# Kernel tuning notes

Hardware: AMD Instinct MI355X
Metric: run time of the kernel (lower is better)

Reference implementation:

```python
import jax, jax.numpy as jnp
import numpy as np

HIDDEN = 1024
HEADS = 16
HEAD_DIM = HIDDEN // HEADS
SCALE = 1.0 / (HEAD_DIM ** 0.5)


def setup_inputs() -> dict:
    key = jax.random.key(0)
    k1, k2, k3 = jax.random.split(key, 3)
    B, S = 2, 2048
    x = jax.random.normal(k1, (B, S, HIDDEN), dtype=jnp.float32)
    # torch Linear weights: (out_features, in_features), y = x @ W.T
    qkv_w = jax.random.normal(k2, (3 * HIDDEN, HIDDEN), dtype=jnp.float32) * (HIDDEN ** -0.5)
    out_w = jax.random.normal(k3, (HIDDEN, HIDDEN), dtype=jnp.float32) * (HIDDEN ** -0.5)
    return {"x": x, "qkv_w": qkv_w, "out_w": out_w}


def reference(x, qkv_w, out_w):
    B, S, H = x.shape
    qkv = jnp.einsum('bsh,oh->bso', x, qkv_w)  # [B,S,3H]
    q, k, v = jnp.split(qkv, 3, axis=-1)
    def heads(t):
        return t.reshape(B, S, HEADS, HEAD_DIM).transpose(0, 2, 1, 3)  # [B,nh,S,hd]
    q, k, v = heads(q), heads(k), heads(v)
    scores = jnp.einsum('bhqd,bhkd->bhqk', q, k) * SCALE  # [B,nh,S,S]
    attn = jax.nn.softmax(scores, axis=-1)
    out = jnp.einsum('bhqk,bhkd->bhqd', attn, v)  # [B,nh,S,hd]
    out = out.transpose(0, 2, 1, 3).reshape(B, S, H)
    return jnp.einsum('bsh,oh->bso', out, out_w)
```

## Files before the change

kernel.cpp:

```cpp
#include <hip/hip_runtime.h>
#include <hip/hip_bf16.h>

#define BB 2
#define SS 2048
#define HH 1024
#define NH 16
#define HD 64
#define MM (BB * SS)
#define N_QKV (3 * HH)
#define KK HH

typedef __attribute__((ext_vector_type(8))) short short8;
typedef __attribute__((ext_vector_type(4))) float floatx4;
typedef __attribute__((ext_vector_type(16))) float floatx16;

#define MFMA16(a, b, c) __builtin_amdgcn_mfma_f32_16x16x32_bf16(a, b, c, 0, 0, 0)
#define MFMA32(a, b, c) __builtin_amdgcn_mfma_f32_32x32x16_bf16(a, b, c, 0, 0, 0)

__device__ __forceinline__ unsigned short f2bf(float f) {
  unsigned int u = __builtin_bit_cast(unsigned int, f);
  u += 0x7FFFu + ((u >> 16) & 1u);
  return (unsigned short)(u >> 16);
}

__device__ __forceinline__ float fexp2(float x) {
#if __has_builtin(__builtin_amdgcn_exp2f)
  return __builtin_amdgcn_exp2f(x);
#else
  float r; asm("v_exp_f32 %0, %1" : "=v"(r) : "v"(x)); return r;
#endif
}

__device__ __forceinline__ unsigned int pack2e(float lo, float hi) {
  unsigned int a = __builtin_bit_cast(unsigned int, lo) + 0x8000u;
  unsigned int b = __builtin_bit_cast(unsigned int, hi) + 0x8000u;
  return __builtin_amdgcn_perm(b, a, 0x07060302u);
}

__device__ __forceinline__ unsigned int cvtpk(float lo, float hi) {
  unsigned int r;
  asm("v_cvt_pk_bf16_f32 %0, %1, %2" : "=v"(r) : "v"(lo), "v"(hi));
  return r;
}

__device__ __forceinline__ uint4 cvt8pk(float4 lo, float4 hi) {
  uint4 u;
  u.x = cvtpk(lo.x, lo.y);
  u.y = cvtpk(lo.z, lo.w);
  u.z = cvtpk(hi.x, hi.y);
  u.w = cvtpk(hi.z, hi.w);
  return u;
}

__device__ __forceinline__ void gload_lds16(const void* g, void* l) {
  __builtin_amdgcn_global_load_lds((const __attribute__((address_space(1))) void*)g,
                                   (__attribute__((address_space(3))) void*)l,
                                   16, 0, 0);
}

__global__ __launch_bounds__(256) void cast_g(const float* __restrict__ s,
                                              unsigned short* __restrict__ d) {
  size_t i = (size_t)blockIdx.x * 256 + threadIdx.x;
  float4 lo = *(const float4*)(s + i * 8);
  float4 hi = *(const float4*)(s + i * 8 + 4);
  *(uint4*)(d + i * 8) = cvt8pk(lo, hi);
}

template <int BPRE>
__global__ __launch_bounds__(256) void gemm_qkv(const unsigned short* __restrict__ Xb,
                                                const float* __restrict__ Wf,
                                                const unsigned short* __restrict__ Wb,
                                                unsigned short* __restrict__ qb,
                                                unsigned short* __restrict__ kb,
                                                unsigned short* __restrict__ vtb) {
  __shared__ __attribute__((aligned(16))) unsigned short As[128 * 32];
  __shared__ __attribute__((aligned(16))) unsigned short Bs[128 * 32];
  const int tid = threadIdx.x;
  const int wave = tid >> 6, lane = tid & 63;
  const int quad = lane >> 4, lc = lane & 15;
  const int m0 = blockIdx.y * 128, n0 = blockIdx.x * 128;
  const int wm = (wave >> 1) * 64, wn = (wave & 1) * 64;
  const int sr = tid >> 2, sc = (tid & 3) * 8;

  floatx4 acc[4][4];
#pragma unroll
  for (int i = 0; i < 4; i++)
#pragma unroll
    for (int j = 0; j < 4; j++) acc[i][j] = (floatx4){0.f, 0.f, 0.f, 0.f};

  const unsigned short* Axp = Xb + (size_t)(m0 + sr) * KK + sc;
  unsigned short* AsD = As + wave * 512;
  unsigned short* BsD = Bs + wave * 512;

  const unsigned short* Bxp = nullptr;
  const float* Bg = nullptr;
  float4 b0l, b0h, b1l, b1h;
  unsigned short* BsW = Bs + wave * 512 + lane * 8;
  if constexpr (BPRE) {
    Bxp = Wb + (size_t)(n0 + sr) * KK + sc;
  } else {
    Bg = Wf + (size_t)(n0 + sr) * KK + sc;
    b0l = *(const float4*)(Bg);                    b0h = *(const float4*)(Bg + 4);
    b1l = *(const float4*)(Bg + (size_t)64 * KK);  b1h = *(const float4*)(Bg + (size_t)64 * KK + 4);
  }

  for (int it = 0; it < KK / 32; ++it) {
    const int k0 = it * 32;
    __syncthreads();
    gload_lds16(Axp + k0, AsD);
    gload_lds16(Axp + (size_t)64 * KK + k0, AsD + 2048);
    if constexpr (BPRE) {
      gload_lds16(Bxp + k0, BsD);
      gload_lds16(Bxp + (size_t)64 * KK + k0, BsD + 2048);
    } else {
      *(uint4*)(BsW) = cvt8pk(b0l, b0h);
      *(uint4*)(BsW + 2048) = cvt8pk(b1l, b1h);
      if (it + 1 < KK / 32) {
        b0l = *(const float4*)(Bg + k0 + 32);                    b0h = *(const float4*)(Bg + k0 + 36);
        b1l = *(const float4*)(Bg + k0 + 32 + (size_t)64 * KK);  b1h = *(const float4*)(Bg + k0 + 36 + (size_t)64 * KK);
      }
    }
    __syncthreads();
    short8 af[4], bf[4];
#pragma unroll
    for (int i = 0; i < 4; i++) {
      af[i] = *(const short8*)(As + (wm + i * 16 + lc) * 32 + quad * 8);
      bf[i] = *(const short8*)(Bs + (wn + i * 16 + lc) * 32 + quad * 8);
    }
#pragma unroll
    for (int i = 0; i < 4; i++)
#pragma unroll
      for (int j = 0; j < 4; j++) acc[i][j] = MFMA16(af[i], bf[j], acc[i][j]);
  }

  const float QSCALE = 0.125f * 1.44269504f;
#pragma unroll
  for (int j = 0; j < 4; j++) {
    int n = n0 + wn + j * 16 + lc;
#pragma unroll
    for (int i = 0; i < 4; i++) {
      int mbase = m0 + wm + i * 16 + quad * 4;
      int b = mbase >> 11;
      int s0 = mbase & 2047;
      if (n < HH) {
        int h = n >> 6, d = n & 63;
#pragma unroll
        for (int r = 0; r < 4; r++)
          qb[(((size_t)(b * NH + h) * SS + s0 + r) * HD) + d] = f2bf(acc[i][j][r] * QSCALE);
      } else if (n < 2 * HH) {
        int n2 = n - HH; int h = n2 >> 6, d = n2 & 63;
#pragma unroll
        for (int r = 0; r < 4; r++)
          kb[(((size_t)(b * NH + h) * SS + s0 + r) * HD) + d] = f2bf(acc[i][j][r]);
      } else {
        int n2 = n - 2 * HH; int h = n2 >> 6, d = n2 & 63;
        ushort4 p;
        p.x = f2bf(acc[i][j][0]); p.y = f2bf(acc[i][j][1]);
        p.z = f2bf(acc[i][j][2]); p.w = f2bf(acc[i][j][3]);
        *(ushort4*)(vtb + ((size_t)(b * NH + h) * HD + d) * SS + s0) = p;
      }
    }
  }
}

__device__ __forceinline__ int co(int row, int c16) {
  return row * 64 + ((c16 ^ ((row ^ (row >> 3)) & 7)) << 3);
}

__global__ __launch_bounds__(256, 2) void attn_kernel(const unsigned short* __restrict__ qg,
                                                      const unsigned short* __restrict__ kg,
                                                      const unsigned short* __restrict__ vtg,
                                                      unsigned short* __restrict__ og) {
  __shared__ __attribute__((aligned(16))) unsigned short Sall[16384];
  unsigned short* Qs = Sall;
  unsigned short* Ks = Sall + 8192;
  unsigned short* Vs = Sall + 12288;

  const int tid = threadIdx.x;
  const int w = tid >> 6, lane = tid & 63;
  const int hl = lane >> 5, c = lane & 31;
  const int q0 = blockIdx.x * 128;
  const int head = blockIdx.y, b = blockIdx.z;

  const unsigned short* qbase = qg + (size_t)(b * NH + head) * SS * HD;
  const unsigned short* kbase = kg + (size_t)(b * NH + head) * SS * HD;
  const unsigned short* vbase = vtg + (size_t)(b * NH + head) * HD * SS;

  {
    int row = tid >> 3, cc = tid & 7;
#pragma unroll
    for (int s = 0; s < 4; s++)
      *(uint4*)(Qs + co(row + 32 * s, cc)) =
          *(const uint4*)(qbase + (size_t)(q0 + row + 32 * s) * HD + cc * 8);
  }

  const int frow = tid >> 3, fc = tid & 7;
  uint4 k0r = *(const uint4*)(kbase + (size_t)frow * HD + fc * 8);
  uint4 k1r = *(const uint4*)(kbase + (size_t)(frow + 32) * HD + fc * 8);
  uint4 v0r = *(const uint4*)(vbase + (size_t)frow * SS + fc * 8);
  uint4 v1r = *(const uint4*)(vbase + (size_t)(frow + 32) * SS + fc * 8);

  floatx16 oacc0, oacc1, lacc;
#pragma unroll
  for (int i = 0; i < 16; i++) { oacc0[i] = 0.f; oacc1[i] = 0.f; lacc[i] = 0.f; }

  short8 ones;
#pragma unroll
  for (int i = 0; i < 8; i++) ones[i] = (short)0x3F80;

  short8 qa[4];

  for (int kt = 0; kt < SS; kt += 64) {
    __syncthreads();
    *(uint4*)(Ks + co(frow, fc)) = k0r;
    *(uint4*)(Ks + co(frow + 32, fc)) = k1r;
    *(uint4*)(Vs + co(frow, fc)) = v0r;
    *(uint4*)(Vs + co(frow + 32, fc)) = v1r;
    if (kt + 64 < SS) {
      k0r = *(const uint4*)(kbase + (size_t)(kt + 64 + frow) * HD + fc * 8);
      k1r = *(const uint4*)(kbase + (size_t)(kt + 96 + frow) * HD + fc * 8);
      v0r = *(const uint4*)(vbase + (size_t)frow * SS + kt + 64 + fc * 8);
      v1r = *(const uint4*)(vbase + (size_t)(frow + 32) * SS + kt + 64 + fc * 8);
    }
    __syncthreads();

    if (kt == 0) {
#pragma unroll
      for (int ks = 0; ks < 4; ks++)
        qa[ks] = *(const short8*)(Qs + co(w * 32 + c, ks * 2 + hl));
    }

    floatx16 sacc0, sacc1;
#pragma unroll
    for (int i = 0; i < 16; i++) { sacc0[i] = 0.f; sacc1[i] = 0.f; }
#pragma unroll
    for (int ks = 0; ks < 4; ks++) {
      short8 ka0 = *(const short8*)(Ks + co(c, ks * 2 + hl));
      short8 ka1 = *(const short8*)(Ks + co(32 + c, ks * 2 + hl));
      sacc0 = MFMA32(ka0, qa[ks], sacc0);
      sacc1 = MFMA32(ka1, qa[ks], sacc1);
    }

    short8 pb[4];
#pragma unroll
    for (int kb = 0; kb < 4; kb++) {
      const floatx16& s = (kb < 2) ? sacc0 : sacc1;
      int base = (kb & 1) * 8;
      unsigned int u0 = pack2e(fexp2(s[base + 0]), fexp2(s[base + 1]));
      unsigned int u1 = pack2e(fexp2(s[base + 2]), fexp2(s[base + 3]));
      unsigned int u2 = pack2e(fexp2(s[base + 4]), fexp2(s[base + 5]));
      unsigned int u3 = pack2e(fexp2(s[base + 6]), fexp2(s[base + 7]));
      uint4 u = {u0, u1, u2, u3};
      pb[kb] = __builtin_bit_cast(short8, u);
    }

#pragma unroll
    for (int kb = 0; kb < 4; kb++) {
      uint2 lo0 = *(const uint2*)(Vs + co(c, 2 * kb) + 4 * hl);
      uint2 hi0 = *(const uint2*)(Vs + co(c, 2 * kb + 1) + 4 * hl);
      uint4 a0 = {lo0.x, lo0.y, hi0.x, hi0.y};
      short8 va0 = __builtin_bit_cast(short8, a0);
      uint2 lo1 = *(const uint2*)(Vs + co(32 + c, 2 * kb) + 4 * hl);
      uint2 hi1 = *(const uint2*)(Vs + co(32 + c, 2 * kb + 1) + 4 * hl);
      uint4 a1 = {lo1.x, lo1.y, hi1.x, hi1.y};
      short8 va1 = __builtin_bit_cast(short8, a1);
      oacc0 = MFMA32(va0, pb[kb], oacc0);
      oacc1 = MFMA32(va1, pb[kb], oacc1);
      lacc = MFMA32(ones, pb[kb], lacc);
    }
  }

  __syncthreads();
  unsigned short* sc = Sall + w * 2176;
  float inv = 1.0f / lacc[0];
#pragma unroll
  for (int t = 0; t < 8; t++) {
    int d0 = ((2 * t) & 3) + 8 * (t >> 1) + 4 * hl;
    *(unsigned int*)(sc + c * 68 + d0) = pack2e(oacc0[2 * t] * inv, oacc0[2 * t + 1] * inv);
    *(unsigned int*)(sc + c * 68 + 32 + d0) = pack2e(oacc1[2 * t] * inv, oacc1[2 * t + 1] * inv);
  }
  {
    int ql = lane >> 1, hf = lane & 1;
    size_t row = (size_t)(b * SS + q0 + w * 32 + ql);
    unsigned short* dst = og + row * HH + head * 64 + hf * 32;
    const unsigned short* srcp = sc + ql * 68 + hf * 32;
#pragma unroll
    for (int s = 0; s < 4; s++) {
      uint2 a = *(const uint2*)(srcp + s * 8);
      uint2 bq = *(const uint2*)(srcp + s * 8 + 4);
      uint4 v = {a.x, a.y, bq.x, bq.y};
      *(uint4*)(dst + s * 8) = v;
    }
  }
}

__global__ __launch_bounds__(256) void gemm_out(const unsigned short* __restrict__ A,
                                                const unsigned short* __restrict__ Wb,
                                                float* __restrict__ C) {
  __shared__ __attribute__((aligned(16))) unsigned short As[128 * 32];
  __shared__ __attribute__((aligned(16))) unsigned short Bs[64 * 32];
  const int tid = threadIdx.x;
  const int wave = tid >> 6, lane = tid & 63;
  const int quad = lane >> 4, lc = lane & 15;
  const int m0 = blockIdx.y * 128, n0 = blockIdx.x * 64;
  const int wm = (wave >> 1) * 64, wn = (wave & 1) * 32;
  const int sr = tid >> 2, sc = (tid & 3) * 8;

  floatx4 acc[4][2];
#pragma unroll
  for (int i = 0; i < 4; i++)
#pragma unroll
    for (int j = 0; j < 2; j++) acc[i][j] = (floatx4){0.f, 0.f, 0.f, 0.f};

  const unsigned short* Axp = A + (size_t)(m0 + sr) * KK + sc;
  const unsigned short* Bxp = Wb + (size_t)(n0 + sr) * KK + sc;
  unsigned short* AsD = As + wave * 512;
  unsigned short* BsD = Bs + wave * 512;

  for (int it = 0; it < KK / 32; ++it) {
    const int k0 = it * 32;
    __syncthreads();
    gload_lds16(Axp + k0, AsD);
    gload_lds16(Axp + (size_t)64 * KK + k0, AsD + 2048);
    gload_lds16(Bxp + k0, BsD);
    __syncthreads();
    short8 af[4], bf[2];
#pragma unroll
    for (int i = 0; i < 4; i++)
      af[i] = *(const short8*)(As + (wm + i * 16 + lc) * 32 + quad * 8);
#pragma unroll
    for (int j = 0; j < 2; j++)
      bf[j] = *(const short8*)(Bs + (wn + j * 16 + lc) * 32 + quad * 8);
#pragma unroll
    for (int i = 0; i < 4; i++)
#pragma unroll
      for (int j = 0; j < 2; j++) acc[i][j] = MFMA16(af[i], bf[j], acc[i][j]);
  }

#pragma unroll
  for (int i = 0; i < 4; i++)
#pragma unroll
    for (int j = 0; j < 2; j++) {
      int m = m0 + wm + i * 16 + quad * 4;
      int n = n0 + wn + j * 16 + lc;
#pragma unroll
      for (int r = 0; r < 4; r++) C[(size_t)(m + r) * HH + n] = acc[i][j][r];
    }
}

extern "C" void kernel_launch(void* const* d_in, const int* in_sizes, int n_in,
                              void* d_out, int out_size, void* d_ws, size_t ws_size,
                              hipStream_t stream) {
  const float* x = (const float*)d_in[0];
  const float* qkv_w = (const float*)d_in[1];
  const float* out_w = (const float*)d_in[2];
  float* out = (float*)d_out;

  char* ws = (char*)d_ws;
  unsigned short* qb  = (unsigned short*)(ws + 0);
  unsigned short* kb  = (unsigned short*)(ws + 8388608);
  unsigned short* vtb = (unsigned short*)(ws + 16777216);
  unsigned short* xb  = (unsigned short*)(ws + 25165824);
  unsigned short* ao  = xb;
  unsigned short* wob = qb;

  const bool big = ws_size >= 40ull * 1024 * 1024;
  unsigned short* w1b = big ? (unsigned short*)(ws + 33554432) : nullptr;

  cast_g<<<dim3(MM * KK / 2048), dim3(256), 0, stream>>>(x, xb);
  if (big) {
    cast_g<<<dim3(N_QKV * KK / 2048), dim3(256), 0, stream>>>(qkv_w, w1b);
    gemm_qkv<1><<<dim3(N_QKV / 128, MM / 128), dim3(256), 0, stream>>>(xb, qkv_w, w1b, qb, kb, vtb);
  } else {
    gemm_qkv<0><<<dim3(N_QKV / 128, MM / 128), dim3(256), 0, stream>>>(xb, qkv_w, nullptr, qb, kb, vtb);
  }
  attn_kernel<<<dim3(SS / 128, NH, BB), dim3(256), 0, stream>>>(qb, kb, vtb, ao);
  cast_g<<<dim3(HH * KK / 2048), dim3(256), 0, stream>>>(out_w, wob);
  gemm_out<<<dim3(HH / 64, MM / 128), dim3(256), 0, stream>>>(ao, wob, out);
}
```

Baseline: 199.7 us.

## Double-buffer LDS in QKV and output GEMMs and fuse input casts

The QKV and output projection GEMMs now use two LDS buffers, issuing the direct global-to-LDS loads for the next K-slice before computing on the current one, with explicit vmcnt waits and barriers in place of two __syncthreads per iteration. This is meant to hide global load latency behind the MFMA work. The x and qkv_w fp32-to-bf16 casts are also merged into one launch on the large-workspace path. Double buffering doubles LDS use per block, which may lower occupancy, and it relies on hand-counted vmcnt values.

```diff
diff --git a/kernel.cpp b/kernel.cpp
--- a/kernel.cpp
+++ b/kernel.cpp
@@ -58,6 +58,20 @@
                                    16, 0, 0);
 }
 
+__global__ __launch_bounds__(256) void cast_xw(const float* __restrict__ x,
+                                               const float* __restrict__ w1,
+                                               unsigned short* __restrict__ xb,
+                                               unsigned short* __restrict__ w1b) {
+  const int NX = MM * KK / 8;
+  int i = blockIdx.x * 256 + threadIdx.x;
+  const float* s; unsigned short* d; int o;
+  if (i < NX) { s = x;  d = xb;  o = i; }
+  else        { s = w1; d = w1b; o = i - NX; }
+  float4 lo = *(const float4*)(s + (size_t)o * 8);
+  float4 hi = *(const float4*)(s + (size_t)o * 8 + 4);
+  *(uint4*)(d + (size_t)o * 8) = cvt8pk(lo, hi);
+}
+
 __global__ __launch_bounds__(256) void cast_g(const float* __restrict__ s,
                                               unsigned short* __restrict__ d) {
   size_t i = (size_t)blockIdx.x * 256 + threadIdx.x;
@@ -66,13 +80,101 @@
   *(uint4*)(d + i * 8) = cvt8pk(lo, hi);
 }
 
-template <int BPRE>
-__global__ __launch_bounds__(256) void gemm_qkv(const unsigned short* __restrict__ Xb,
-                                                const float* __restrict__ Wf,
-                                                const unsigned short* __restrict__ Wb,
-                                                unsigned short* __restrict__ qb,
-                                                unsigned short* __restrict__ kb,
-                                                unsigned short* __restrict__ vtb) {
+__global__ __launch_bounds__(256) void gemm_qkv_dma(const unsigned short* __restrict__ Xb,
+                                                    const unsigned short* __restrict__ Wb,
+                                                    unsigned short* __restrict__ qb,
+                                                    unsigned short* __restrict__ kb,
+                                                    unsigned short* __restrict__ vtb) {
+  __shared__ __attribute__((aligned(16))) unsigned short As[2][128 * 32];
+  __shared__ __attribute__((aligned(16))) unsigned short Bs[2][128 * 32];
+  const int tid = threadIdx.x;
+  const int wave = tid >> 6;
+  const int lane = tid & 63;
+  const int quad = lane >> 4, lc = lane & 15;
+  const int m0 = blockIdx.y * 128, n0 = blockIdx.x * 128;
+  const int wm = (wave >> 1) * 64, wn = (wave & 1) * 64;
+  const int sr = tid >> 2, sc = (tid & 3) * 8;
+
+  floatx4 acc[4][4];
+#pragma unroll
+  for (int i = 0; i < 4; i++)
+#pragma unroll
+    for (int j = 0; j < 4; j++) acc[i][j] = (floatx4){0.f, 0.f, 0.f, 0.f};
+
+  const unsigned short* Axp = Xb + (size_t)(m0 + sr) * KK + sc;
+  const unsigned short* Bxp = Wb + (size_t)(n0 + sr) * KK + sc;
+
+#define STAGEQ(buf, k0)                                               \
+  do {                                                                \
+    gload_lds16(Axp + (k0), &As[buf][wave * 512]);                    \
+    gload_lds16(Axp + (size_t)64 * KK + (k0), &As[buf][wave * 512 + 2048]); \
+    gload_lds16(Bxp + (k0), &Bs[buf][wave * 512]);                    \
+    gload_lds16(Bxp + (size_t)64 * KK + (k0), &Bs[buf][wave * 512 + 2048]); \
+  } while (0)
+
+  STAGEQ(0, 0);
+
+  const int NIT = KK / 32;
+  for (int it = 0; it < NIT; ++it) {
+    const int cb = it & 1;
+    if (it + 1 < NIT) {
+      STAGEQ(cb ^ 1, (it + 1) * 32);
+      asm volatile("s_waitcnt vmcnt(4)" ::: "memory");
+    } else {
+      asm volatile("s_waitcnt vmcnt(0)" ::: "memory");
+    }
+    __builtin_amdgcn_s_barrier();
+    __builtin_amdgcn_sched_barrier(0);
+    short8 af[4], bfr[4];
+#pragma unroll
+    for (int i = 0; i < 4; i++) {
+      af[i]  = *(const short8*)(&As[cb][(wm + i * 16 + lc) * 32 + quad * 8]);
+      bfr[i] = *(const short8*)(&Bs[cb][(wn + i * 16 + lc) * 32 + quad * 8]);
+    }
+#pragma unroll
+    for (int i = 0; i < 4; i++)
+#pragma unroll
+      for (int j = 0; j < 4; j++) acc[i][j] = MFMA16(af[i], bfr[j], acc[i][j]);
+    __builtin_amdgcn_sched_barrier(0);
+    __builtin_amdgcn_s_barrier();
+  }
+#undef STAGEQ
+
+  const float QSCALE = 0.125f * 1.44269504f;
+#pragma unroll
+  for (int j = 0; j < 4; j++) {
+    int n = n0 + wn + j * 16 + lc;
+#pragma unroll
+    for (int i = 0; i < 4; i++) {
+      int mbase = m0 + wm + i * 16 + quad * 4;
+      int b = mbase >> 11;
+      int s0 = mbase & 2047;
+      if (n < HH) {
+        int h = n >> 6, d = n & 63;
+#pragma unroll
+        for (int r = 0; r < 4; r++)
+          qb[(((size_t)(b * NH + h) * SS + s0 + r) * HD) + d] = f2bf(acc[i][j][r] * QSCALE);
+      } else if (n < 2 * HH) {
+        int n2 = n - HH; int h = n2 >> 6, d = n2 & 63;
+#pragma unroll
+        for (int r = 0; r < 4; r++)
+          kb[(((size_t)(b * NH + h) * SS + s0 + r) * HD) + d] = f2bf(acc[i][j][r]);
+      } else {
+        int n2 = n - 2 * HH; int h = n2 >> 6, d = n2 & 63;
+        ushort4 p;
+        p.x = f2bf(acc[i][j][0]); p.y = f2bf(acc[i][j][1]);
+        p.z = f2bf(acc[i][j][2]); p.w = f2bf(acc[i][j][3]);
+        *(ushort4*)(vtb + ((size_t)(b * NH + h) * HD + d) * SS + s0) = p;
+      }
+    }
+  }
+}
+
+__global__ __launch_bounds__(256) void gemm_qkv_f32(const unsigned short* __restrict__ Xb,
+                                                    const float* __restrict__ Wf,
+                                                    unsigned short* __restrict__ qb,
+                                                    unsigned short* __restrict__ kb,
+                                                    unsigned short* __restrict__ vtb) {
   __shared__ __attribute__((aligned(16))) unsigned short As[128 * 32];
   __shared__ __attribute__((aligned(16))) unsigned short Bs[128 * 32];
   const int tid = threadIdx.x;
@@ -90,47 +192,33 @@
 
   const unsigned short* Axp = Xb + (size_t)(m0 + sr) * KK + sc;
   unsigned short* AsD = As + wave * 512;
-  unsigned short* BsD = Bs + wave * 512;
-
-  const unsigned short* Bxp = nullptr;
-  const float* Bg = nullptr;
-  float4 b0l, b0h, b1l, b1h;
+  const float* Bg = Wf + (size_t)(n0 + sr) * KK + sc;
   unsigned short* BsW = Bs + wave * 512 + lane * 8;
-  if constexpr (BPRE) {
-    Bxp = Wb + (size_t)(n0 + sr) * KK + sc;
-  } else {
-    Bg = Wf + (size_t)(n0 + sr) * KK + sc;
-    b0l = *(const float4*)(Bg);                    b0h = *(const float4*)(Bg + 4);
-    b1l = *(const float4*)(Bg + (size_t)64 * KK);  b1h = *(const float4*)(Bg + (size_t)64 * KK + 4);
-  }
+  float4 b0l = *(const float4*)(Bg),                    b0h = *(const float4*)(Bg + 4);
+  float4 b1l = *(const float4*)(Bg + (size_t)64 * KK),  b1h = *(const float4*)(Bg + (size_t)64 * KK + 4);
 
   for (int it = 0; it < KK / 32; ++it) {
     const int k0 = it * 32;
     __syncthreads();
     gload_lds16(Axp + k0, AsD);
     gload_lds16(Axp + (size_t)64 * KK + k0, AsD + 2048);
-    if constexpr (BPRE) {
-      gload_lds16(Bxp + k0, BsD);
-      gload_lds16(Bxp + (size_t)64 * KK + k0, BsD + 2048);
-    } else {
-      *(uint4*)(BsW) = cvt8pk(b0l, b0h);
-      *(uint4*)(BsW + 2048) = cvt8pk(b1l, b1h);
-      if (it + 1 < KK / 32) {
-        b0l = *(const float4*)(Bg + k0 + 32);                    b0h = *(const float4*)(Bg + k0 + 36);
-        b1l = *(const float4*)(Bg + k0 + 32 + (size_t)64 * KK);  b1h = *(const float4*)(Bg + k0 + 36 + (size_t)64 * KK);
-      }
+    *(uint4*)(BsW) = cvt8pk(b0l, b0h);
+    *(uint4*)(BsW + 2048) = cvt8pk(b1l, b1h);
+    if (it + 1 < KK / 32) {
+      b0l = *(const float4*)(Bg + k0 + 32);                    b0h = *(const float4*)(Bg + k0 + 36);
+      b1l = *(const float4*)(Bg + k0 + 32 + (size_t)64 * KK);  b1h = *(const float4*)(Bg + k0 + 36 + (size_t)64 * KK);
     }
     __syncthreads();
-    short8 af[4], bf[4];
+    short8 af[4], bfr[4];
 #pragma unroll
     for (int i = 0; i < 4; i++) {
-      af[i] = *(const short8*)(As + (wm + i * 16 + lc) * 32 + quad * 8);
-      bf[i] = *(const short8*)(Bs + (wn + i * 16 + lc) * 32 + quad * 8);
+      af[i]  = *(const short8*)(As + (wm + i * 16 + lc) * 32 + quad * 8);
+      bfr[i] = *(const short8*)(Bs + (wn + i * 16 + lc) * 32 + quad * 8);
     }
 #pragma unroll
     for (int i = 0; i < 4; i++)
 #pragma unroll
-      for (int j = 0; j < 4; j++) acc[i][j] = MFMA16(af[i], bf[j], acc[i][j]);
+      for (int j = 0; j < 4; j++) acc[i][j] = MFMA16(af[i], bfr[j], acc[i][j]);
   }
 
   const float QSCALE = 0.125f * 1.44269504f;
@@ -294,11 +382,11 @@
   }
 }
 
-__global__ __launch_bounds__(256) void gemm_out(const unsigned short* __restrict__ A,
-                                                const unsigned short* __restrict__ Wb,
-                                                float* __restrict__ C) {
-  __shared__ __attribute__((aligned(16))) unsigned short As[128 * 32];
-  __shared__ __attribute__((aligned(16))) unsigned short Bs[64 * 32];
+__global__ __launch_bounds__(256) void gemm_out_dma(const unsigned short* __restrict__ A,
+                                                    const unsigned short* __restrict__ Wb,
+                                                    float* __restrict__ C) {
+  __shared__ __attribute__((aligned(16))) unsigned short As[2][128 * 32];
+  __shared__ __attribute__((aligned(16))) unsigned short Bs[2][64 * 32];
   const int tid = threadIdx.x;
   const int wave = tid >> 6, lane = tid & 63;
   const int quad = lane >> 4, lc = lane & 15;
@@ -314,28 +402,42 @@
 
   const unsigned short* Axp = A + (size_t)(m0 + sr) * KK + sc;
   const unsigned short* Bxp = Wb + (size_t)(n0 + sr) * KK + sc;
-  unsigned short* AsD = As + wave * 512;
-  unsigned short* BsD = Bs + wave * 512;
-
-  for (int it = 0; it < KK / 32; ++it) {
-    const int k0 = it * 32;
-    __syncthreads();
-    gload_lds16(Axp + k0, AsD);
-    gload_lds16(Axp + (size_t)64 * KK + k0, AsD + 2048);
-    gload_lds16(Bxp + k0, BsD);
-    __syncthreads();
-    short8 af[4], bf[2];
+
+#define STAGEO(buf, k0)                                               \
+  do {                                                                \
+    gload_lds16(Axp + (k0), &As[buf][wave * 512]);                    \
+    gload_lds16(Axp + (size_t)64 * KK + (k0), &As[buf][wave * 512 + 2048]); \
+    gload_lds16(Bxp + (k0), &Bs[buf][wave * 512]);                    \
+  } while (0)
+
+  STAGEO(0, 0);
+
+  const int NIT = KK / 32;
+  for (int it = 0; it < NIT; ++it) {
+    const int cb = it & 1;
+    if (it + 1 < NIT) {
+      STAGEO(cb ^ 1, (it + 1) * 32);
+      asm volatile("s_waitcnt vmcnt(3)" ::: "memory");
+    } else {
+      asm volatile("s_waitcnt vmcnt(0)" ::: "memory");
+    }
+    __builtin_amdgcn_s_barrier();
+    __builtin_amdgcn_sched_barrier(0);
+    short8 af[4], bfr[2];
 #pragma unroll
     for (int i = 0; i < 4; i++)
-      af[i] = *(const short8*)(As + (wm + i * 16 + lc) * 32 + quad * 8);
+      af[i] = *(const short8*)(&As[cb][(wm + i * 16 + lc) * 32 + quad * 8]);
 #pragma unroll
     for (int j = 0; j < 2; j++)
-      bf[j] = *(const short8*)(Bs + (wn + j * 16 + lc) * 32 + quad * 8);
+      bfr[j] = *(const short8*)(&Bs[cb][(wn + j * 16 + lc) * 32 + quad * 8]);
 #pragma unroll
     for (int i = 0; i < 4; i++)
 #pragma unroll
-      for (int j = 0; j < 2; j++) acc[i][j] = MFMA16(af[i], bf[j], acc[i][j]);
-  }
+      for (int j = 0; j < 2; j++) acc[i][j] = MFMA16(af[i], bfr[j], acc[i][j]);
+    __builtin_amdgcn_sched_barrier(0);
+    __builtin_amdgcn_s_barrier();
+  }
+#undef STAGEO
 
 #pragma unroll
   for (int i = 0; i < 4; i++)
@@ -367,14 +469,14 @@
   const bool big = ws_size >= 40ull * 1024 * 1024;
   unsigned short* w1b = big ? (unsigned short*)(ws + 33554432) : nullptr;
 
-  cast_g<<<dim3(MM * KK / 2048), dim3(256), 0, stream>>>(x, xb);
   if (big) {
-    cast_g<<<dim3(N_QKV * KK / 2048), dim3(256), 0, stream>>>(qkv_w, w1b);
-    gemm_qkv<1><<<dim3(N_QKV / 128, MM / 128), dim3(256), 0, stream>>>(xb, qkv_w, w1b, qb, kb, vtb);
+    cast_xw<<<dim3((MM * KK + N_QKV * KK) / 2048), dim3(256), 0, stream>>>(x, qkv_w, xb, w1b);
+    gemm_qkv_dma<<<dim3(N_QKV / 128, MM / 128), dim3(256), 0, stream>>>(xb, w1b, qb, kb, vtb);
   } else {
-    gemm_qkv<0><<<dim3(N_QKV / 128, MM / 128), dim3(256), 0, stream>>>(xb, qkv_w, nullptr, qb, kb, vtb);
+    cast_g<<<dim3(MM * KK / 2048), dim3(256), 0, stream>>>(x, xb);
+    gemm_qkv_f32<<<dim3(N_QKV / 128, MM / 128), dim3(256), 0, stream>>>(xb, qkv_w, qb, kb, vtb);
   }
   attn_kernel<<<dim3(SS / 128, NH, BB), dim3(256), 0, stream>>>(qb, kb, vtb, ao);
   cast_g<<<dim3(HH * KK / 2048), dim3(256), 0, stream>>>(out_w, wob);
-  gemm_out<<<dim3(HH / 64, MM / 128), dim3(256), 0, stream>>>(ao, wob, out);
-}
+  gemm_out_dma<<<dim3(HH / 64, MM / 128), dim3(256), 0, stream>>>(ao, wob, out);
+}
```

New measurement: 192.6 us. 3.6% less time.
